# Performance work log

Hardware: AMD Instinct MI355X
Metric: run time of the kernel (lower is better)

## Reference

```python
import jax, jax.numpy as jnp
import numpy as np

B, N, C = 2, 6, 80
FH, FW = 16, 44
D = 112
NX = NY = 128
NZ = 1
OGH, OGW = 256, 704
D_BOUND = (2.0, 58.0, 0.5)
VOXEL_SIZE = np.array([0.8, 0.8, 8.0], dtype=np.float32)
VOXEL_COORD = np.array([-51.2 + 0.4, -51.2 + 0.4, -5.0 + 4.0], dtype=np.float32)
VOXEL_NUM = np.array([NX, NY, NZ], dtype=np.int32)


def setup_inputs() -> dict:
    key = jax.random.key(0)
    k1, k2 = jax.random.split(key)
    context = jax.random.normal(k1, (B * N, C, FH, FW), jnp.float32)
    depth_logits = jax.random.normal(k2, (B * N, D, FH, FW), jnp.float32)
    # realistic camera matrices (random matrices would not be invertible / physical)
    intrin = np.tile(np.eye(4, dtype=np.float32), (B, N, 1, 1))
    intrin[..., 0, 0] = 560.0
    intrin[..., 1, 1] = 560.0
    intrin[..., 0, 2] = OGW / 2.0
    intrin[..., 1, 2] = OGH / 2.0
    ida = np.tile(np.eye(4, dtype=np.float32), (B, N, 1, 1))
    s2e = np.tile(np.eye(4, dtype=np.float32), (B, N, 1, 1))
    # cam axes (x right, y down, z forward) -> ego axes (x fwd, y left, z up)
    M = np.array([[0., 0., 1.], [-1., 0., 0.], [0., -1., 0.]], dtype=np.float32)
    for n in range(N):
        yaw = 2.0 * np.pi * n / N
        cy, sy = np.cos(yaw), np.sin(yaw)
        R = np.array([[cy, -sy, 0.], [sy, cy, 0.], [0., 0., 1.]], dtype=np.float32)
        s2e[:, n, :3, :3] = R @ M
        s2e[:, n, :3, 3] = np.array([1.5 * cy, 1.5 * sy, 1.6], dtype=np.float32)
    bda = np.tile(np.eye(4, dtype=np.float32), (B, 1, 1))
    return dict(context=context, depth_logits=depth_logits,
                sensor2ego_mat=jnp.asarray(s2e), intrin_mat=jnp.asarray(intrin),
                ida_mat=jnp.asarray(ida), bda_mat=jnp.asarray(bda))


def _frustum():
    # [D, FH, FW, 4] pixel-plane frustum: (u, v, depth, 1)
    d = jnp.arange(D_BOUND[0], D_BOUND[1], D_BOUND[2], dtype=jnp.float32) + D_BOUND[2] / 2.0
    d = jnp.broadcast_to(d[:, None, None], (D, FH, FW))
    xs = jnp.broadcast_to(jnp.linspace(0.0, OGW - 1.0, FW)[None, None, :], (D, FH, FW))
    ys = jnp.broadcast_to(jnp.linspace(0.0, OGH - 1.0, FH)[None, :, None], (D, FH, FW))
    return jnp.stack([xs, ys, d, jnp.ones_like(d)], -1)


def reference(context, depth_logits, sensor2ego_mat, intrin_mat, ida_mat, bda_mat):
    # ---- get_geometry ----
    pts = _frustum()[None, None, ..., None]                       # [1,1,D,FH,FW,4,1]
    ida_inv = jnp.linalg.inv(ida_mat).reshape(B, N, 1, 1, 1, 4, 4)
    pts = ida_inv @ pts
    pts = jnp.concatenate([pts[..., :2, :] * pts[..., 2:3, :], pts[..., 2:, :]], axis=-2)
    combine = (sensor2ego_mat @ jnp.linalg.inv(intrin_mat)).reshape(B, N, 1, 1, 1, 4, 4)
    pts = combine @ pts
    bda = bda_mat.reshape(B, 1, 1, 1, 1, 4, 4)
    geom = (bda @ pts)[..., :3, 0]                                # [B,N,D,FH,FW,3] ego coords

    # ---- voxel indices ----
    vsize = jnp.asarray(VOXEL_SIZE)
    vcoord = jnp.asarray(VOXEL_COORD)
    vnum = jnp.asarray(VOXEL_NUM)
    idx = jnp.floor((geom - (vcoord - vsize / 2.0)) / vsize).astype(jnp.int32)
    valid = jnp.all((idx >= 0) & (idx < vnum), axis=-1)           # [B,N,D,FH,FW]

    # ---- lift: depth-weighted outer product ----
    depth = jax.nn.softmax(depth_logits, axis=1).reshape(B, N, D, FH, FW)
    ctx = context.reshape(B, N, C, FH, FW)
    feat = jnp.einsum('bndhw,bnchw->bndhwc', depth, ctx)          # [B,N,D,FH,FW,C]
    feat = feat * valid[..., None]

    # ---- splat: scatter-add into BEV grid ----
    b_idx = jnp.arange(B, dtype=jnp.int32)[:, None, None, None, None]
    lin = b_idx * (NY * NX) + idx[..., 1] * NX + idx[..., 0]
    lin = jnp.where(valid, lin, 0)                                # invalid feats already zeroed
    bev = jax.ops.segment_sum(feat.reshape(-1, C), lin.reshape(-1),
                              num_segments=B * NY * NX)
    return bev.reshape(B, NY, NX, C).transpose(0, 3, 1, 2)        # [B,C,NY,NX]
```

## Files before the change

### kernel.cpp

```cpp
#include <hip/hip_runtime.h>
#include <hip/hip_bf16.h>
#include <math.h>

#define B_ 2
#define N_ 6
#define C_ 80
#define FH_ 16
#define FW_ 44
#define D_ 112
#define NX_ 128
#define NY_ 128
#define NCOL (B_ * N_ * FH_ * FW_)
#define NCELL (B_ * NY_ * NX_)
#define MAXT (NCOL * D_)
#define GB_CELLS 16

typedef __hip_bfloat16 bf16;
typedef unsigned short u16;

__device__ __forceinline__ float loadf(const void* p, int i, int isbf) {
  if (isbf) return __bfloat162float(((const bf16*)p)[i]);
  return ((const float*)p)[i];
}

__device__ void inv4(const float m[16], float invOut[16]) {
  float inv[16];
  inv[0]  =  m[5]*m[10]*m[15] - m[5]*m[11]*m[14] - m[9]*m[6]*m[15] + m[9]*m[7]*m[14] + m[13]*m[6]*m[11] - m[13]*m[7]*m[10];
  inv[4]  = -m[4]*m[10]*m[15] + m[4]*m[11]*m[14] + m[8]*m[6]*m[15] - m[8]*m[7]*m[14] - m[12]*m[6]*m[11] + m[12]*m[7]*m[10];
  inv[8]  =  m[4]*m[9]*m[15]  - m[4]*m[11]*m[13] - m[8]*m[5]*m[15] + m[8]*m[7]*m[13] + m[12]*m[5]*m[11] - m[12]*m[7]*m[9];
  inv[12] = -m[4]*m[9]*m[14]  + m[4]*m[10]*m[13] + m[8]*m[5]*m[14] - m[8]*m[6]*m[13] - m[12]*m[5]*m[10] + m[12]*m[6]*m[9];
  inv[1]  = -m[1]*m[10]*m[15] + m[1]*m[11]*m[14] + m[9]*m[2]*m[15] - m[9]*m[3]*m[14] - m[13]*m[2]*m[11] + m[13]*m[3]*m[10];
  inv[5]  =  m[0]*m[10]*m[15] - m[0]*m[11]*m[14] - m[8]*m[2]*m[15] + m[8]*m[3]*m[14] + m[12]*m[2]*m[11] - m[12]*m[3]*m[10];
  inv[9]  = -m[0]*m[9]*m[15]  + m[0]*m[11]*m[13] + m[8]*m[1]*m[15] - m[8]*m[3]*m[13] - m[12]*m[1]*m[11] + m[12]*m[3]*m[9];
  inv[13] =  m[0]*m[9]*m[14]  - m[0]*m[10]*m[13] - m[8]*m[1]*m[14] + m[8]*m[2]*m[13] + m[12]*m[1]*m[10] - m[12]*m[2]*m[9];
  inv[2]  =  m[1]*m[6]*m[15]  - m[1]*m[7]*m[14]  - m[5]*m[2]*m[15] + m[5]*m[3]*m[14] + m[13]*m[2]*m[7]  - m[13]*m[3]*m[6];
  inv[6]  = -m[0]*m[6]*m[15]  + m[0]*m[7]*m[14]  + m[4]*m[2]*m[15] - m[4]*m[3]*m[14] - m[12]*m[2]*m[7]  + m[12]*m[3]*m[6];
  inv[10] =  m[0]*m[5]*m[15]  - m[0]*m[7]*m[13]  - m[4]*m[1]*m[15] + m[4]*m[3]*m[13] + m[12]*m[1]*m[7]  - m[12]*m[3]*m[5];
  inv[14] = -m[0]*m[5]*m[14]  + m[0]*m[6]*m[13]  + m[4]*m[1]*m[14] - m[4]*m[2]*m[13] - m[12]*m[1]*m[6]  + m[12]*m[2]*m[5];
  inv[3]  = -m[1]*m[6]*m[11]  + m[1]*m[7]*m[10]  + m[5]*m[2]*m[11] - m[5]*m[3]*m[10] - m[9]*m[2]*m[7]   + m[9]*m[3]*m[6];
  inv[7]  =  m[0]*m[6]*m[11]  - m[0]*m[7]*m[10]  - m[4]*m[2]*m[11] + m[4]*m[3]*m[10] + m[8]*m[2]*m[7]   - m[8]*m[3]*m[6];
  inv[11] = -m[0]*m[5]*m[11]  + m[0]*m[7]*m[9]   + m[4]*m[1]*m[11] - m[4]*m[3]*m[9]  - m[8]*m[1]*m[7]   + m[8]*m[3]*m[5];
  inv[15] =  m[0]*m[5]*m[10]  - m[0]*m[6]*m[9]   - m[4]*m[1]*m[10] + m[4]*m[2]*m[9]  + m[8]*m[1]*m[6]   - m[8]*m[2]*m[5];
  float det = m[0]*inv[0] + m[1]*inv[4] + m[2]*inv[8] + m[3]*inv[12];
  det = 1.0f / det;
  for (int i = 0; i < 16; i++) invOut[i] = inv[i] * det;
}

__device__ void mul4(const float A[16], const float Bm[16], float Cm[16]) {
  for (int i = 0; i < 4; i++)
    for (int j = 0; j < 4; j++) {
      float s = 0.f;
      for (int k = 0; k < 4; k++) s += A[i * 4 + k] * Bm[k * 4 + j];
      Cm[i * 4 + j] = s;
    }
}

__global__ void lss_prep(const void* __restrict__ logits,
                         const void* __restrict__ s2e, const void* __restrict__ intrin,
                         const void* __restrict__ ida, const void* __restrict__ bda,
                         float* __restrict__ mats, int* __restrict__ flags) {
  __shared__ int s_cnt;
  __shared__ int s_mats_bf;
  const int t = threadIdx.x;
  if (t == 0) s_cnt = 0;
  __syncthreads();
  {
    const unsigned short* u = (const unsigned short*)logits;
    unsigned short v = u[2 * t];
    int e = (v >> 7) & 0xFF;
    if (v == 0 || (e >= 110 && e <= 136)) atomicAdd(&s_cnt, 1);
  }
  __syncthreads();
  if (t == 0) {
    flags[0] = (s_cnt > 170) ? 1 : 0;
    float v = ((const float*)intrin)[0];
    s_mats_bf = (v > 100.f && v < 1.0e6f) ? 0 : 1;
    flags[1] = s_mats_bf;
  }
  __syncthreads();
  const int mbf = s_mats_bf;
  if (t < B_ * N_) {
    int b = t / N_;
    float S[16], I[16], A[16], Bd[16], Iinv[16], Ainv[16], Cm[16], M[16];
    for (int i = 0; i < 16; i++) {
      S[i]  = loadf(s2e,    t * 16 + i, mbf);
      I[i]  = loadf(intrin, t * 16 + i, mbf);
      A[i]  = loadf(ida,    t * 16 + i, mbf);
      Bd[i] = loadf(bda,    b * 16 + i, mbf);
    }
    inv4(I, Iinv);
    inv4(A, Ainv);
    mul4(S, Iinv, Cm);
    mul4(Bd, Cm, M);
    for (int i = 0; i < 16; i++) { mats[t * 32 + i] = Ainv[i]; mats[t * 32 + 16 + i] = M[i]; }
  }
}

__global__ void lss_transpose(const void* __restrict__ ctx, const int* __restrict__ flags,
                              float* __restrict__ ctx_t) {
  int i = blockIdx.x * blockDim.x + threadIdx.x;
  if (i >= NCOL * C_) return;
  int col = i / C_, c = i - col * C_;
  int bn = col / (FH_ * FW_), r = col - bn * (FH_ * FW_);
  int h = r / FW_, w = r - h * FW_;
  ctx_t[i] = loadf(ctx, ((bn * C_ + c) * FH_ + h) * FW_ + w, flags[0]);
}

__device__ __forceinline__ int geom_cell(const float* __restrict__ mats,
                                         int bn, int h, int w, int d) {
  const float* Ai = mats + bn * 32;
  const float* M = mats + bn * 32 + 16;
  float u = (float)w * (703.0f / 43.0f);
  float v = (float)h * 17.0f;
  float dep = 2.25f + 0.5f * (float)d;
  float p0 = ((Ai[0] * u + Ai[1] * v) + Ai[2] * dep) + Ai[3];
  float p1 = ((Ai[4] * u + Ai[5] * v) + Ai[6] * dep) + Ai[7];
  float p2 = ((Ai[8] * u + Ai[9] * v) + Ai[10] * dep) + Ai[11];
  float p3 = ((Ai[12] * u + Ai[13] * v) + Ai[14] * dep) + Ai[15];
  float q0 = p0 * p2, q1 = p1 * p2;
  float gx = ((M[0] * q0 + M[1] * q1) + M[2] * p2) + M[3] * p3;
  float gy = ((M[4] * q0 + M[5] * q1) + M[6] * p2) + M[7] * p3;
  float gz = ((M[8] * q0 + M[9] * q1) + M[10] * p2) + M[11] * p3;
  int ix = (int)floorf((gx + 51.2f) / 0.8f);
  int iy = (int)floorf((gy + 51.2f) / 0.8f);
  int iz = (int)floorf((gz + 5.0f) / 8.0f);
  bool valid = (ix >= 0) && (ix < NX_) && (iy >= 0) && (iy < NY_) && (iz == 0);
  int b = bn / N_;
  return valid ? (b * (NY_ * NX_) + iy * NX_ + ix) : -1;
}

__global__ __launch_bounds__(64) void lss_count(const float* __restrict__ mats,
                                                int* __restrict__ counts) {
  const int tid = threadIdx.x;
  const int col = blockIdx.x;
  const int w = col % FW_;
  const int h = (col / FW_) % FH_;
  const int bn = col / (FW_ * FH_);
  __shared__ int s_cell[D_];
  s_cell[tid] = geom_cell(mats, bn, h, w, tid);
  if (tid < D_ - 64) s_cell[tid + 64] = geom_cell(mats, bn, h, w, tid + 64);
  __syncthreads();
  for (int d = tid; d < D_; d += 64) {
    int vcell = s_cell[d];
    if (vcell >= 0 && (d == 0 || s_cell[d - 1] != vcell)) atomicAdd(&counts[vcell], 1);
  }
}

__global__ __launch_bounds__(1024) void lss_scan(const int* __restrict__ counts,
                                                 int* __restrict__ offsets,
                                                 int* __restrict__ cursors) {
  __shared__ int s[1024];
  const int t = threadIdx.x;
  const int base = t * 32;
  int local[32];
  int sum = 0;
  for (int j = 0; j < 32; j++) { local[j] = counts[base + j]; sum += local[j]; }
  s[t] = sum;
  __syncthreads();
  for (int st = 1; st < 1024; st <<= 1) {
    int v = (t >= st) ? s[t - st] : 0;
    __syncthreads();
    s[t] += v;
    __syncthreads();
  }
  int run = s[t] - sum;
  for (int j = 0; j < 32; j++) {
    offsets[base + j] = run;
    cursors[base + j] = run;
    run += local[j];
  }
}

__global__ __launch_bounds__(64) void lss_fill(
    const void* __restrict__ logits, const float* __restrict__ mats,
    const int* __restrict__ flags, int* __restrict__ cursors,
    u16* __restrict__ colids, float* __restrict__ wts) {
  const int tid = threadIdx.x;
  const int col = blockIdx.x;
  const int w = col % FW_;
  const int h = (col / FW_) % FH_;
  const int bn = col / (FW_ * FH_);
  const int tbf = flags[0];

  __shared__ float s_w[D_];
  __shared__ int s_cell[D_];

  const int base = ((bn * D_) * FH_ + h) * FW_ + w;
  float l0 = loadf(logits, base + tid * (FH_ * FW_), tbf);
  float l1 = (tid < D_ - 64) ? loadf(logits, base + (tid + 64) * (FH_ * FW_), tbf) : -1e30f;
  float m = fmaxf(l0, l1);
  for (int s = 32; s > 0; s >>= 1) m = fmaxf(m, __shfl_xor(m, s));
  float e0 = expf(l0 - m);
  float e1 = (tid < D_ - 64) ? expf(l1 - m) : 0.f;
  float sum = e0 + e1;
  for (int s = 32; s > 0; s >>= 1) sum += __shfl_xor(sum, s);
  float inv_sum = 1.0f / sum;

  s_w[tid] = e0;
  s_cell[tid] = geom_cell(mats, bn, h, w, tid);
  if (tid < D_ - 64) {
    s_w[tid + 64] = e1;
    s_cell[tid + 64] = geom_cell(mats, bn, h, w, tid + 64);
  }
  __syncthreads();

  for (int d = tid; d < D_; d += 64) {
    int vcell = s_cell[d];
    if (vcell >= 0 && (d == 0 || s_cell[d - 1] != vcell)) {
      float acc = s_w[d];
      for (int j = d + 1; j < D_ && s_cell[j] == vcell; ++j) acc += s_w[j];
      int pos = atomicAdd(&cursors[vcell], 1);
      colids[pos] = (u16)col;
      wts[pos] = acc * inv_sum;
    }
  }
}

__global__ __launch_bounds__(1024) void lss_gather(
    const float* __restrict__ ctx_t, const int* __restrict__ counts,
    const int* __restrict__ offsets, const u16* __restrict__ colids,
    const float* __restrict__ wts, const int* __restrict__ flags,
    void* __restrict__ out) {
  __shared__ float s_out[GB_CELLS * 84];
  const int tid = threadIdx.x;
  const int wv = tid >> 6;
  const int ln = tid & 63;
  const int sl = ln >> 2;
  const int g = ln & 3;
  const int cell = blockIdx.x * GB_CELLS + wv;
  const int n = counts[cell];
  const int off = offsets[cell];

  float acc[20];
#pragma unroll
  for (int i = 0; i < 20; i++) acc[i] = 0.f;

  for (int j = sl; j < n; j += 16) {
    int colj = colids[off + j];
    float wj = wts[off + j];
    const float4* cp = (const float4*)(ctx_t + colj * C_ + g * 20);
#pragma unroll
    for (int q = 0; q < 5; q++) {
      float4 v = cp[q];
      acc[q * 4 + 0] += wj * v.x;
      acc[q * 4 + 1] += wj * v.y;
      acc[q * 4 + 2] += wj * v.z;
      acc[q * 4 + 3] += wj * v.w;
    }
  }
#pragma unroll
  for (int msk = 4; msk <= 32; msk <<= 1) {
#pragma unroll
    for (int i = 0; i < 20; i++) acc[i] += __shfl_xor(acc[i], msk);
  }
  if (sl == 0) {
#pragma unroll
    for (int i = 0; i < 20; i++) s_out[wv * 84 + g * 20 + i] = acc[i];
  }
  __syncthreads();

  const int x = tid & 15;
  const int c0 = tid >> 4;
  const int cell0 = blockIdx.x * GB_CELLS;
  const int b = cell0 >> 14;
  const int yx0 = cell0 & 16383;
  if (flags[0]) {
    bf16* o = (bf16*)out;
    o[(size_t)(b * C_ + c0) * (NY_ * NX_) + yx0 + x] = __float2bfloat16(s_out[x * 84 + c0]);
    if (c0 < 16)
      o[(size_t)(b * C_ + 64 + c0) * (NY_ * NX_) + yx0 + x] = __float2bfloat16(s_out[x * 84 + 64 + c0]);
  } else {
    float* o = (float*)out;
    o[(size_t)(b * C_ + c0) * (NY_ * NX_) + yx0 + x] = s_out[x * 84 + c0];
    if (c0 < 16)
      o[(size_t)(b * C_ + 64 + c0) * (NY_ * NX_) + yx0 + x] = s_out[x * 84 + 64 + c0];
  }
}

extern "C" void kernel_launch(void* const* d_in, const int* in_sizes, int n_in,
                              void* d_out, int out_size, void* d_ws, size_t ws_size,
                              hipStream_t stream) {
  const void* ctx = d_in[0];
  const void* logits = d_in[1];
  const void* s2e = d_in[2];
  const void* intrin = d_in[3];
  const void* ida = d_in[4];
  const void* bda = d_in[5];

  float* wsf = (float*)d_ws;
  int* flags   = (int*)wsf;
  float* mats  = wsf + 16;
  int* counts  = (int*)(wsf + 512);
  int* offsets = (int*)(wsf + 512 + NCELL);
  int* cursors = (int*)(wsf + 512 + 2 * NCELL);
  float* ctx_t = wsf + 512 + 3 * NCELL;
  u16* colids  = (u16*)(ctx_t + NCOL * C_);
  float* wts   = (float*)((float*)colids + MAXT / 2);

  hipMemsetAsync(counts, 0, NCELL * sizeof(int), stream);
  lss_prep<<<1, 256, 0, stream>>>(logits, s2e, intrin, ida, bda, mats, flags);
  lss_transpose<<<(NCOL * C_ + 255) / 256, 256, 0, stream>>>(ctx, flags, ctx_t);
  lss_count<<<NCOL, 64, 0, stream>>>(mats, counts);
  lss_scan<<<1, 1024, 0, stream>>>(counts, offsets, cursors);
  lss_fill<<<NCOL, 64, 0, stream>>>(logits, mats, flags, cursors, colids, wts);
  lss_gather<<<NCELL / GB_CELLS, 1024, 0, stream>>>(ctx_t, counts, offsets, colids, wts, flags, d_out);
}
```

Baseline: 193.5 us.

## Fuse prep, transpose, count, scan and fill into one cooperative kernel

Replaces the memset and the five front-end launches (prep, transpose, count, scan, fill) with a single cooperative kernel that uses grid-wide syncs between phases. The counting phase now works per wavefront with shuffles, and the single-block scan becomes a two-level scan: per-chunk wave scans followed by a block scan of the chunk sums. The aim is to remove per-launch overhead and the serial single-block scan. In exchange it adds several grid barriers and runs on a grid capped at 512 blocks, so each wave handles several columns in a loop.

```diff
diff --git a/kernel.cpp b/kernel.cpp
--- a/kernel.cpp
+++ b/kernel.cpp
@@ -1,6 +1,9 @@
 #include <hip/hip_runtime.h>
+#include <hip/hip_cooperative_groups.h>
 #include <hip/hip_bf16.h>
 #include <math.h>
+
+namespace cg = cooperative_groups;
 
 #define B_ 2
 #define N_ 6
@@ -14,6 +17,7 @@
 #define NCELL (B_ * NY_ * NX_)
 #define MAXT (NCOL * D_)
 #define GB_CELLS 16
+#define NCHUNK (NCELL / 64)
 
 typedef __hip_bfloat16 bf16;
 typedef unsigned short u16;
@@ -55,57 +59,6 @@
     }
 }
 
-__global__ void lss_prep(const void* __restrict__ logits,
-                         const void* __restrict__ s2e, const void* __restrict__ intrin,
-                         const void* __restrict__ ida, const void* __restrict__ bda,
-                         float* __restrict__ mats, int* __restrict__ flags) {
-  __shared__ int s_cnt;
-  __shared__ int s_mats_bf;
-  const int t = threadIdx.x;
-  if (t == 0) s_cnt = 0;
-  __syncthreads();
-  {
-    const unsigned short* u = (const unsigned short*)logits;
-    unsigned short v = u[2 * t];
-    int e = (v >> 7) & 0xFF;
-    if (v == 0 || (e >= 110 && e <= 136)) atomicAdd(&s_cnt, 1);
-  }
-  __syncthreads();
-  if (t == 0) {
-    flags[0] = (s_cnt > 170) ? 1 : 0;
-    float v = ((const float*)intrin)[0];
-    s_mats_bf = (v > 100.f && v < 1.0e6f) ? 0 : 1;
-    flags[1] = s_mats_bf;
-  }
-  __syncthreads();
-  const int mbf = s_mats_bf;
-  if (t < B_ * N_) {
-    int b = t / N_;
-    float S[16], I[16], A[16], Bd[16], Iinv[16], Ainv[16], Cm[16], M[16];
-    for (int i = 0; i < 16; i++) {
-      S[i]  = loadf(s2e,    t * 16 + i, mbf);
-      I[i]  = loadf(intrin, t * 16 + i, mbf);
-      A[i]  = loadf(ida,    t * 16 + i, mbf);
-      Bd[i] = loadf(bda,    b * 16 + i, mbf);
-    }
-    inv4(I, Iinv);
-    inv4(A, Ainv);
-    mul4(S, Iinv, Cm);
-    mul4(Bd, Cm, M);
-    for (int i = 0; i < 16; i++) { mats[t * 32 + i] = Ainv[i]; mats[t * 32 + 16 + i] = M[i]; }
-  }
-}
-
-__global__ void lss_transpose(const void* __restrict__ ctx, const int* __restrict__ flags,
-                              float* __restrict__ ctx_t) {
-  int i = blockIdx.x * blockDim.x + threadIdx.x;
-  if (i >= NCOL * C_) return;
-  int col = i / C_, c = i - col * C_;
-  int bn = col / (FH_ * FW_), r = col - bn * (FH_ * FW_);
-  int h = r / FW_, w = r - h * FW_;
-  ctx_t[i] = loadf(ctx, ((bn * C_ + c) * FH_ + h) * FW_ + w, flags[0]);
-}
-
 __device__ __forceinline__ int geom_cell(const float* __restrict__ mats,
                                          int bn, int h, int w, int d) {
   const float* Ai = mats + bn * 32;
@@ -129,90 +82,169 @@
   return valid ? (b * (NY_ * NX_) + iy * NX_ + ix) : -1;
 }
 
-__global__ __launch_bounds__(64) void lss_count(const float* __restrict__ mats,
-                                                int* __restrict__ counts) {
-  const int tid = threadIdx.x;
-  const int col = blockIdx.x;
-  const int w = col % FW_;
-  const int h = (col / FW_) % FH_;
-  const int bn = col / (FW_ * FH_);
-  __shared__ int s_cell[D_];
-  s_cell[tid] = geom_cell(mats, bn, h, w, tid);
-  if (tid < D_ - 64) s_cell[tid + 64] = geom_cell(mats, bn, h, w, tid + 64);
-  __syncthreads();
-  for (int d = tid; d < D_; d += 64) {
-    int vcell = s_cell[d];
-    if (vcell >= 0 && (d == 0 || s_cell[d - 1] != vcell)) atomicAdd(&counts[vcell], 1);
-  }
-}
-
-__global__ __launch_bounds__(1024) void lss_scan(const int* __restrict__ counts,
-                                                 int* __restrict__ offsets,
-                                                 int* __restrict__ cursors) {
-  __shared__ int s[1024];
+__global__ __launch_bounds__(256, 2) void lss_front(
+    const void* __restrict__ ctx, const void* __restrict__ logits,
+    const void* __restrict__ s2e, const void* __restrict__ intrin,
+    const void* __restrict__ ida, const void* __restrict__ bda,
+    float* __restrict__ mats, int* __restrict__ flags,
+    int* __restrict__ counts, int* __restrict__ offsets,
+    int* __restrict__ cursors, float* __restrict__ ctx_t,
+    u16* __restrict__ colids, float* __restrict__ wts,
+    int* __restrict__ bsum, int* __restrict__ boff) {
+  cg::grid_group grid = cg::this_grid();
   const int t = threadIdx.x;
-  const int base = t * 32;
-  int local[32];
-  int sum = 0;
-  for (int j = 0; j < 32; j++) { local[j] = counts[base + j]; sum += local[j]; }
-  s[t] = sum;
-  __syncthreads();
-  for (int st = 1; st < 1024; st <<= 1) {
-    int v = (t >= st) ? s[t - st] : 0;
-    __syncthreads();
-    s[t] += v;
-    __syncthreads();
-  }
-  int run = s[t] - sum;
-  for (int j = 0; j < 32; j++) {
-    offsets[base + j] = run;
-    cursors[base + j] = run;
-    run += local[j];
-  }
-}
-
-__global__ __launch_bounds__(64) void lss_fill(
-    const void* __restrict__ logits, const float* __restrict__ mats,
-    const int* __restrict__ flags, int* __restrict__ cursors,
-    u16* __restrict__ colids, float* __restrict__ wts) {
-  const int tid = threadIdx.x;
-  const int col = blockIdx.x;
-  const int w = col % FW_;
-  const int h = (col / FW_) % FH_;
-  const int bn = col / (FW_ * FH_);
+  const int blk = blockIdx.x;
+  const int nblk = gridDim.x;
+  const int gtid = blk * 256 + t;
+  const int nthr = nblk * 256;
+  const int ln = t & 63;
+  const int wv = t >> 6;
+  const int gw = blk * 4 + wv;
+  const int ngw = nblk * 4;
+
+  __shared__ float s_w[4][D_];
+  __shared__ int s_cell[4][D_];
+  __shared__ int s_scan[256];
+  __shared__ int s_misc[2];
+
+  for (int i = gtid; i < NCELL; i += nthr) counts[i] = 0;
+  if (blk == 0) {
+    if (t == 0) s_misc[0] = 0;
+    __syncthreads();
+    {
+      const unsigned short* u = (const unsigned short*)logits;
+      unsigned short v = u[2 * t];
+      int e = (v >> 7) & 0xFF;
+      if (v == 0 || (e >= 110 && e <= 136)) atomicAdd(&s_misc[0], 1);
+    }
+    __syncthreads();
+    if (t == 0) {
+      flags[0] = (s_misc[0] > 170) ? 1 : 0;
+      float v = ((const float*)intrin)[0];
+      s_misc[1] = (v > 100.f && v < 1.0e6f) ? 0 : 1;
+      flags[1] = s_misc[1];
+    }
+    __syncthreads();
+    const int mbf = s_misc[1];
+    if (t < B_ * N_) {
+      int b = t / N_;
+      float S[16], I[16], A[16], Bd[16], Iinv[16], Ainv[16], Cm[16], M[16];
+      for (int i = 0; i < 16; i++) {
+        S[i]  = loadf(s2e,    t * 16 + i, mbf);
+        I[i]  = loadf(intrin, t * 16 + i, mbf);
+        A[i]  = loadf(ida,    t * 16 + i, mbf);
+        Bd[i] = loadf(bda,    b * 16 + i, mbf);
+      }
+      inv4(I, Iinv);
+      inv4(A, Ainv);
+      mul4(S, Iinv, Cm);
+      mul4(Bd, Cm, M);
+      for (int i = 0; i < 16; i++) { mats[t * 32 + i] = Ainv[i]; mats[t * 32 + 16 + i] = M[i]; }
+    }
+  }
+  grid.sync();
+
   const int tbf = flags[0];
-
-  __shared__ float s_w[D_];
-  __shared__ int s_cell[D_];
-
-  const int base = ((bn * D_) * FH_ + h) * FW_ + w;
-  float l0 = loadf(logits, base + tid * (FH_ * FW_), tbf);
-  float l1 = (tid < D_ - 64) ? loadf(logits, base + (tid + 64) * (FH_ * FW_), tbf) : -1e30f;
-  float m = fmaxf(l0, l1);
-  for (int s = 32; s > 0; s >>= 1) m = fmaxf(m, __shfl_xor(m, s));
-  float e0 = expf(l0 - m);
-  float e1 = (tid < D_ - 64) ? expf(l1 - m) : 0.f;
-  float sum = e0 + e1;
-  for (int s = 32; s > 0; s >>= 1) sum += __shfl_xor(sum, s);
-  float inv_sum = 1.0f / sum;
-
-  s_w[tid] = e0;
-  s_cell[tid] = geom_cell(mats, bn, h, w, tid);
-  if (tid < D_ - 64) {
-    s_w[tid + 64] = e1;
-    s_cell[tid + 64] = geom_cell(mats, bn, h, w, tid + 64);
-  }
-  __syncthreads();
-
-  for (int d = tid; d < D_; d += 64) {
-    int vcell = s_cell[d];
-    if (vcell >= 0 && (d == 0 || s_cell[d - 1] != vcell)) {
-      float acc = s_w[d];
-      for (int j = d + 1; j < D_ && s_cell[j] == vcell; ++j) acc += s_w[j];
-      int pos = atomicAdd(&cursors[vcell], 1);
-      colids[pos] = (u16)col;
-      wts[pos] = acc * inv_sum;
-    }
+  for (int i = gtid; i < NCOL * C_; i += nthr) {
+    int col = i / C_, c = i - col * C_;
+    int bn = col / (FH_ * FW_), r = col - bn * (FH_ * FW_);
+    int h = r / FW_, w = r - h * FW_;
+    ctx_t[i] = loadf(ctx, ((bn * C_ + c) * FH_ + h) * FW_ + w, tbf);
+  }
+  for (int col = gw; col < NCOL; col += ngw) {
+    const int w = col % FW_;
+    const int h = (col / FW_) % FH_;
+    const int bn = col / (FW_ * FH_);
+    int c0 = geom_cell(mats, bn, h, w, ln);
+    int c1 = (ln < D_ - 64) ? geom_cell(mats, bn, h, w, ln + 64) : -3;
+    int p0 = __shfl_up(c0, 1);
+    int p1 = __shfl_up(c1, 1);
+    int c63 = __shfl(c0, 63);
+    if (ln == 0) p1 = c63;
+    if (c0 >= 0 && (ln == 0 || p0 != c0)) atomicAdd(&counts[c0], 1);
+    if (c1 >= 0 && p1 != c1) atomicAdd(&counts[c1], 1);
+  }
+  grid.sync();
+
+  for (int cb = gw; cb < NCHUNK; cb += ngw) {
+    int c = cb * 64 + ln;
+    int v = counts[c];
+    int incl = v;
+#pragma unroll
+    for (int s = 1; s < 64; s <<= 1) {
+      int u2 = __shfl_up(incl, s);
+      if (ln >= s) incl += u2;
+    }
+    offsets[c] = incl - v;
+    if (ln == 63) bsum[cb] = incl;
+  }
+  grid.sync();
+
+  if (blk == 0) {
+    int a  = bsum[2 * t];
+    int b2 = bsum[2 * t + 1];
+    int ps = a + b2;
+    s_scan[t] = ps;
+    __syncthreads();
+    for (int st = 1; st < 256; st <<= 1) {
+      int u2 = (t >= st) ? s_scan[t - st] : 0;
+      __syncthreads();
+      s_scan[t] += u2;
+      __syncthreads();
+    }
+    int base = s_scan[t] - ps;
+    boff[2 * t]     = base;
+    boff[2 * t + 1] = base + a;
+  }
+  grid.sync();
+
+  for (int i = gtid; i < NCELL; i += nthr) {
+    int off = offsets[i] + boff[i >> 6];
+    offsets[i] = off;
+    cursors[i] = off;
+  }
+  grid.sync();
+
+  const int ITER = (NCOL + ngw - 1) / ngw;
+  for (int it = 0; it < ITER; ++it) {
+    const int col = gw + it * ngw;
+    const bool act = col < NCOL;
+    float inv_sum = 0.f;
+    if (act) {
+      const int w = col % FW_;
+      const int h = (col / FW_) % FH_;
+      const int bn = col / (FW_ * FH_);
+      const int base = ((bn * D_) * FH_ + h) * FW_ + w;
+      float l0 = loadf(logits, base + ln * (FH_ * FW_), tbf);
+      float l1 = (ln < D_ - 64) ? loadf(logits, base + (ln + 64) * (FH_ * FW_), tbf) : -1e30f;
+      float m = fmaxf(l0, l1);
+      for (int s = 32; s > 0; s >>= 1) m = fmaxf(m, __shfl_xor(m, s));
+      float e0 = expf(l0 - m);
+      float e1 = (ln < D_ - 64) ? expf(l1 - m) : 0.f;
+      float sum = e0 + e1;
+      for (int s = 32; s > 0; s >>= 1) sum += __shfl_xor(sum, s);
+      inv_sum = 1.0f / sum;
+      s_w[wv][ln] = e0;
+      s_cell[wv][ln] = geom_cell(mats, bn, h, w, ln);
+      if (ln < D_ - 64) {
+        s_w[wv][ln + 64] = e1;
+        s_cell[wv][ln + 64] = geom_cell(mats, bn, h, w, ln + 64);
+      }
+    }
+    __syncthreads();
+    if (act) {
+      for (int d = ln; d < D_; d += 64) {
+        int vcell = s_cell[wv][d];
+        if (vcell >= 0 && (d == 0 || s_cell[wv][d - 1] != vcell)) {
+          float acc = s_w[wv][d];
+          for (int j = d + 1; j < D_ && s_cell[wv][j] == vcell; ++j) acc += s_w[wv][j];
+          int pos = atomicAdd(&cursors[vcell], 1);
+          colids[pos] = (u16)col;
+          wts[pos] = acc * inv_sum;
+        }
+      }
+    }
+    __syncthreads();
   }
 }
 
@@ -293,15 +325,33 @@
   int* counts  = (int*)(wsf + 512);
   int* offsets = (int*)(wsf + 512 + NCELL);
   int* cursors = (int*)(wsf + 512 + 2 * NCELL);
-  float* ctx_t = wsf + 512 + 3 * NCELL;
+  int* bsum    = (int*)(wsf + 512 + 3 * NCELL);
+  int* boff    = bsum + NCHUNK;
+  float* ctx_t = wsf + 512 + 3 * NCELL + 2 * NCHUNK;
   u16* colids  = (u16*)(ctx_t + NCOL * C_);
   float* wts   = (float*)((float*)colids + MAXT / 2);
 
-  hipMemsetAsync(counts, 0, NCELL * sizeof(int), stream);
-  lss_prep<<<1, 256, 0, stream>>>(logits, s2e, intrin, ida, bda, mats, flags);
-  lss_transpose<<<(NCOL * C_ + 255) / 256, 256, 0, stream>>>(ctx, flags, ctx_t);
-  lss_count<<<NCOL, 64, 0, stream>>>(mats, counts);
-  lss_scan<<<1, 1024, 0, stream>>>(counts, offsets, cursors);
-  lss_fill<<<NCOL, 64, 0, stream>>>(logits, mats, flags, cursors, colids, wts);
-  lss_gather<<<NCELL / GB_CELLS, 1024, 0, stream>>>(ctx_t, counts, offsets, colids, wts, flags, d_out);
-}
+  static int grid_blocks = 0;
+  if (grid_blocks == 0) {
+    int nb = 0;
+    hipOccupancyMaxActiveBlocksPerMultiprocessor(&nb, (const void*)lss_front, 256, 0);
+    if (nb < 1) nb = 1;
+    long g = (long)nb * 256;
+    grid_blocks = (int)(g < 512 ? g : 512);
+  }
+
+  void* args[16];
+  args[0] = (void*)&ctx;     args[1] = (void*)&logits;
+  args[2] = (void*)&s2e;     args[3] = (void*)&intrin;
+  args[4] = (void*)&ida;     args[5] = (void*)&bda;
+  args[6] = (void*)&mats;    args[7] = (void*)&flags;
+  args[8] = (void*)&counts;  args[9] = (void*)&offsets;
+  args[10] = (void*)&cursors; args[11] = (void*)&ctx_t;
+  args[12] = (void*)&colids; args[13] = (void*)&wts;
+  args[14] = (void*)&bsum;   args[15] = (void*)&boff;
+
+  hipLaunchCooperativeKernel((void*)lss_front, dim3(grid_blocks), dim3(256),
+                             args, 0, stream);
+  lss_gather<<<NCELL / GB_CELLS, 1024, 0, stream>>>(ctx_t, counts, offsets,
+                                                    colids, wts, flags, d_out);
+}
```

Measured after the change: 316.8 us. 63.8% more time.

## Fuse count, scan, fill and transpose into one build kernel plus scatter

Applied to the files above, without the earlier changes.

Replaces the memset, transpose, count, scan and fill kernels with one build kernel. In it, some blocks transpose context and others compute softmax and voxel runs per column, one thread per column. A last-block-done atomic lets the final block run the prefix scan, and a separate scatter kernel places the precomputed runs into cell buckets. This cuts launches and avoids computing geometry twice, but adds per-column serial loops over depth with strided logit loads, extra run buffers, and a scan done by a single block.

```diff
diff --git a/kernel.cpp b/kernel.cpp
--- a/kernel.cpp
+++ b/kernel.cpp
@@ -10,10 +10,12 @@
 #define D_ 112
 #define NX_ 128
 #define NY_ 128
-#define NCOL (B_ * N_ * FH_ * FW_)
+#define HW_ (FH_ * FW_)
+#define NCOL (B_ * N_ * HW_)
 #define NCELL (B_ * NY_ * NX_)
 #define MAXT (NCOL * D_)
 #define GB_CELLS 16
+#define NBB 256
 
 typedef __hip_bfloat16 bf16;
 typedef unsigned short u16;
@@ -55,57 +57,6 @@
     }
 }
 
-__global__ void lss_prep(const void* __restrict__ logits,
-                         const void* __restrict__ s2e, const void* __restrict__ intrin,
-                         const void* __restrict__ ida, const void* __restrict__ bda,
-                         float* __restrict__ mats, int* __restrict__ flags) {
-  __shared__ int s_cnt;
-  __shared__ int s_mats_bf;
-  const int t = threadIdx.x;
-  if (t == 0) s_cnt = 0;
-  __syncthreads();
-  {
-    const unsigned short* u = (const unsigned short*)logits;
-    unsigned short v = u[2 * t];
-    int e = (v >> 7) & 0xFF;
-    if (v == 0 || (e >= 110 && e <= 136)) atomicAdd(&s_cnt, 1);
-  }
-  __syncthreads();
-  if (t == 0) {
-    flags[0] = (s_cnt > 170) ? 1 : 0;
-    float v = ((const float*)intrin)[0];
-    s_mats_bf = (v > 100.f && v < 1.0e6f) ? 0 : 1;
-    flags[1] = s_mats_bf;
-  }
-  __syncthreads();
-  const int mbf = s_mats_bf;
-  if (t < B_ * N_) {
-    int b = t / N_;
-    float S[16], I[16], A[16], Bd[16], Iinv[16], Ainv[16], Cm[16], M[16];
-    for (int i = 0; i < 16; i++) {
-      S[i]  = loadf(s2e,    t * 16 + i, mbf);
-      I[i]  = loadf(intrin, t * 16 + i, mbf);
-      A[i]  = loadf(ida,    t * 16 + i, mbf);
-      Bd[i] = loadf(bda,    b * 16 + i, mbf);
-    }
-    inv4(I, Iinv);
-    inv4(A, Ainv);
-    mul4(S, Iinv, Cm);
-    mul4(Bd, Cm, M);
-    for (int i = 0; i < 16; i++) { mats[t * 32 + i] = Ainv[i]; mats[t * 32 + 16 + i] = M[i]; }
-  }
-}
-
-__global__ void lss_transpose(const void* __restrict__ ctx, const int* __restrict__ flags,
-                              float* __restrict__ ctx_t) {
-  int i = blockIdx.x * blockDim.x + threadIdx.x;
-  if (i >= NCOL * C_) return;
-  int col = i / C_, c = i - col * C_;
-  int bn = col / (FH_ * FW_), r = col - bn * (FH_ * FW_);
-  int h = r / FW_, w = r - h * FW_;
-  ctx_t[i] = loadf(ctx, ((bn * C_ + c) * FH_ + h) * FW_ + w, flags[0]);
-}
-
 __device__ __forceinline__ int geom_cell(const float* __restrict__ mats,
                                          int bn, int h, int w, int d) {
   const float* Ai = mats + bn * 32;
@@ -129,90 +80,149 @@
   return valid ? (b * (NY_ * NX_) + iy * NX_ + ix) : -1;
 }
 
-__global__ __launch_bounds__(64) void lss_count(const float* __restrict__ mats,
-                                                int* __restrict__ counts) {
-  const int tid = threadIdx.x;
-  const int col = blockIdx.x;
-  const int w = col % FW_;
-  const int h = (col / FW_) % FH_;
-  const int bn = col / (FW_ * FH_);
-  __shared__ int s_cell[D_];
-  s_cell[tid] = geom_cell(mats, bn, h, w, tid);
-  if (tid < D_ - 64) s_cell[tid + 64] = geom_cell(mats, bn, h, w, tid + 64);
-  __syncthreads();
-  for (int d = tid; d < D_; d += 64) {
-    int vcell = s_cell[d];
-    if (vcell >= 0 && (d == 0 || s_cell[d - 1] != vcell)) atomicAdd(&counts[vcell], 1);
-  }
-}
-
-__global__ __launch_bounds__(1024) void lss_scan(const int* __restrict__ counts,
-                                                 int* __restrict__ offsets,
-                                                 int* __restrict__ cursors) {
-  __shared__ int s[1024];
+__global__ void lss_prep(const void* __restrict__ logits,
+                         const void* __restrict__ s2e, const void* __restrict__ intrin,
+                         const void* __restrict__ ida, const void* __restrict__ bda,
+                         float* __restrict__ mats, int* __restrict__ flags,
+                         int* __restrict__ counts, int* __restrict__ done) {
+  __shared__ int s_cnt;
+  __shared__ int s_mats_bf;
   const int t = threadIdx.x;
-  const int base = t * 32;
-  int local[32];
-  int sum = 0;
-  for (int j = 0; j < 32; j++) { local[j] = counts[base + j]; sum += local[j]; }
-  s[t] = sum;
-  __syncthreads();
-  for (int st = 1; st < 1024; st <<= 1) {
-    int v = (t >= st) ? s[t - st] : 0;
+  if (t == 0) { s_cnt = 0; *done = 0; }
+  __syncthreads();
+  {
+    const unsigned short* u = (const unsigned short*)logits;
+    unsigned short v = u[2 * t];
+    int e = (v >> 7) & 0xFF;
+    if (v == 0 || (e >= 110 && e <= 136)) atomicAdd(&s_cnt, 1);
+  }
+  __syncthreads();
+  if (t == 0) {
+    flags[0] = (s_cnt > 170) ? 1 : 0;
+    float v = ((const float*)intrin)[0];
+    s_mats_bf = (v > 100.f && v < 1.0e6f) ? 0 : 1;
+    flags[1] = s_mats_bf;
+  }
+  __syncthreads();
+  const int mbf = s_mats_bf;
+  if (t < B_ * N_) {
+    int b = t / N_;
+    float S[16], I[16], A[16], Bd[16], Iinv[16], Ainv[16], Cm[16], M[16];
+    for (int i = 0; i < 16; i++) {
+      S[i]  = loadf(s2e,    t * 16 + i, mbf);
+      I[i]  = loadf(intrin, t * 16 + i, mbf);
+      A[i]  = loadf(ida,    t * 16 + i, mbf);
+      Bd[i] = loadf(bda,    b * 16 + i, mbf);
+    }
+    inv4(I, Iinv);
+    inv4(A, Ainv);
+    mul4(S, Iinv, Cm);
+    mul4(Bd, Cm, M);
+    for (int i = 0; i < 16; i++) { mats[t * 32 + i] = Ainv[i]; mats[t * 32 + 16 + i] = M[i]; }
+  }
+  for (int i = t; i < NCELL; i += 256) counts[i] = 0;
+}
+
+__global__ __launch_bounds__(256) void lss_build(
+    const void* __restrict__ ctx, const void* __restrict__ logits,
+    const float* __restrict__ mats, const int* __restrict__ flags,
+    int* __restrict__ counts, int* __restrict__ offsets, int* __restrict__ cursors,
+    int* __restrict__ done, int* __restrict__ nrun,
+    u16* __restrict__ runc, float* __restrict__ runw, float* __restrict__ ctx_t) {
+  const int t = threadIdx.x;
+  const int blk = blockIdx.x;
+  const int tbf = flags[0];
+
+  if (blk >= 33) {
+    for (int i = (blk - 33) * 256 + t; i < NCOL * C_; i += (NBB - 33) * 256) {
+      int bn = i / (C_ * HW_);
+      int r  = i - bn * (C_ * HW_);
+      int c  = r / HW_;
+      int hw = r - c * HW_;
+      ctx_t[(bn * HW_ + hw) * C_ + c] = loadf(ctx, i, tbf);
+    }
+  } else {
+    const int col = blk * 256 + t;
+    const int bn = col / HW_;
+    const int hw = col - bn * HW_;
+    const int h = hw / FW_, w = hw - h * FW_;
+    const int base = bn * (D_ * HW_) + hw;
+    float m = -1e30f, s = 0.f;
+    for (int d = 0; d < D_; ++d) {
+      float l = loadf(logits, base + d * HW_, tbf);
+      float nm = fmaxf(m, l);
+      s = s * expf(m - nm) + expf(l - nm);
+      m = nm;
+    }
+    const float inv_sum = 1.0f / s;
+    int prev = -1; float racc = 0.f; int nr = 0;
+    for (int d = 0; d < D_; ++d) {
+      float l = loadf(logits, base + d * HW_, tbf);
+      float wgt = expf(l - m) * inv_sum;
+      int cell = geom_cell(mats, bn, h, w, d);
+      if (cell != prev) {
+        if (prev >= 0) {
+          runc[col * D_ + nr] = (u16)prev; runw[col * D_ + nr] = racc; ++nr;
+          atomicAdd(&counts[prev], 1);
+        }
+        prev = cell; racc = wgt;
+      } else {
+        racc += wgt;
+      }
+    }
+    if (prev >= 0) {
+      runc[col * D_ + nr] = (u16)prev; runw[col * D_ + nr] = racc; ++nr;
+      atomicAdd(&counts[prev], 1);
+    }
+    nrun[col] = nr;
+  }
+
+  __syncthreads();
+  __shared__ int s_last;
+  if (t == 0) {
+    __threadfence();
+    s_last = (atomicAdd(done, 1) == NBB - 1);
+  }
+  __syncthreads();
+  if (!s_last) return;
+  __threadfence();
+
+  __shared__ int s_sum[256];
+  const int cb = t * 128;
+  int tot = 0;
+  for (int j = 0; j < 128; ++j)
+    tot += __hip_atomic_load(&counts[cb + j], __ATOMIC_RELAXED, __HIP_MEMORY_SCOPE_AGENT);
+  s_sum[t] = tot;
+  __syncthreads();
+  for (int st = 1; st < 256; st <<= 1) {
+    int v = (t >= st) ? s_sum[t - st] : 0;
     __syncthreads();
-    s[t] += v;
+    s_sum[t] += v;
     __syncthreads();
   }
-  int run = s[t] - sum;
-  for (int j = 0; j < 32; j++) {
-    offsets[base + j] = run;
-    cursors[base + j] = run;
-    run += local[j];
-  }
-}
-
-__global__ __launch_bounds__(64) void lss_fill(
-    const void* __restrict__ logits, const float* __restrict__ mats,
-    const int* __restrict__ flags, int* __restrict__ cursors,
+  int run = s_sum[t] - tot;
+  for (int j = 0; j < 128; ++j) {
+    int v = __hip_atomic_load(&counts[cb + j], __ATOMIC_RELAXED, __HIP_MEMORY_SCOPE_AGENT);
+    offsets[cb + j] = run;
+    cursors[cb + j] = run;
+    run += v;
+  }
+}
+
+__global__ __launch_bounds__(256) void lss_scatter(
+    const int* __restrict__ nrun, const u16* __restrict__ runc,
+    const float* __restrict__ runw, int* __restrict__ cursors,
     u16* __restrict__ colids, float* __restrict__ wts) {
-  const int tid = threadIdx.x;
-  const int col = blockIdx.x;
-  const int w = col % FW_;
-  const int h = (col / FW_) % FH_;
-  const int bn = col / (FW_ * FH_);
-  const int tbf = flags[0];
-
-  __shared__ float s_w[D_];
-  __shared__ int s_cell[D_];
-
-  const int base = ((bn * D_) * FH_ + h) * FW_ + w;
-  float l0 = loadf(logits, base + tid * (FH_ * FW_), tbf);
-  float l1 = (tid < D_ - 64) ? loadf(logits, base + (tid + 64) * (FH_ * FW_), tbf) : -1e30f;
-  float m = fmaxf(l0, l1);
-  for (int s = 32; s > 0; s >>= 1) m = fmaxf(m, __shfl_xor(m, s));
-  float e0 = expf(l0 - m);
-  float e1 = (tid < D_ - 64) ? expf(l1 - m) : 0.f;
-  float sum = e0 + e1;
-  for (int s = 32; s > 0; s >>= 1) sum += __shfl_xor(sum, s);
-  float inv_sum = 1.0f / sum;
-
-  s_w[tid] = e0;
-  s_cell[tid] = geom_cell(mats, bn, h, w, tid);
-  if (tid < D_ - 64) {
-    s_w[tid + 64] = e1;
-    s_cell[tid + 64] = geom_cell(mats, bn, h, w, tid + 64);
-  }
-  __syncthreads();
-
-  for (int d = tid; d < D_; d += 64) {
-    int vcell = s_cell[d];
-    if (vcell >= 0 && (d == 0 || s_cell[d - 1] != vcell)) {
-      float acc = s_w[d];
-      for (int j = d + 1; j < D_ && s_cell[j] == vcell; ++j) acc += s_w[j];
-      int pos = atomicAdd(&cursors[vcell], 1);
-      colids[pos] = (u16)col;
-      wts[pos] = acc * inv_sum;
-    }
+  const int col = blockIdx.x * 4 + (threadIdx.x >> 6);
+  const int ln = threadIdx.x & 63;
+  if (col >= NCOL) return;
+  const int nr = nrun[col];
+  for (int r = ln; r < nr; r += 64) {
+    int cell = runc[col * D_ + r];
+    float wv = runw[col * D_ + r];
+    int pos = atomicAdd(&cursors[cell], 1);
+    colids[pos] = (u16)col;
+    wts[pos] = wv;
   }
 }
 
@@ -289,19 +299,21 @@
 
   float* wsf = (float*)d_ws;
   int* flags   = (int*)wsf;
+  int* done    = flags + 4;
   float* mats  = wsf + 16;
   int* counts  = (int*)(wsf + 512);
-  int* offsets = (int*)(wsf + 512 + NCELL);
-  int* cursors = (int*)(wsf + 512 + 2 * NCELL);
-  float* ctx_t = wsf + 512 + 3 * NCELL;
-  u16* colids  = (u16*)(ctx_t + NCOL * C_);
-  float* wts   = (float*)((float*)colids + MAXT / 2);
-
-  hipMemsetAsync(counts, 0, NCELL * sizeof(int), stream);
-  lss_prep<<<1, 256, 0, stream>>>(logits, s2e, intrin, ida, bda, mats, flags);
-  lss_transpose<<<(NCOL * C_ + 255) / 256, 256, 0, stream>>>(ctx, flags, ctx_t);
-  lss_count<<<NCOL, 64, 0, stream>>>(mats, counts);
-  lss_scan<<<1, 1024, 0, stream>>>(counts, offsets, cursors);
-  lss_fill<<<NCOL, 64, 0, stream>>>(logits, mats, flags, cursors, colids, wts);
+  int* offsets = counts + NCELL;
+  int* cursors = offsets + NCELL;
+  int* nrun    = cursors + NCELL;
+  float* runw  = (float*)(nrun + NCOL);
+  float* ctx_t = runw + MAXT;
+  float* wts   = ctx_t + NCOL * C_;
+  u16* colids  = (u16*)(wts + MAXT);
+  u16* runc    = colids + MAXT;
+
+  lss_prep<<<1, 256, 0, stream>>>(logits, s2e, intrin, ida, bda, mats, flags, counts, done);
+  lss_build<<<NBB, 256, 0, stream>>>(ctx, logits, mats, flags, counts, offsets,
+                                     cursors, done, nrun, runc, runw, ctx_t);
+  lss_scatter<<<NCOL / 4, 256, 0, stream>>>(nrun, runc, runw, cursors, colids, wts);
   lss_gather<<<NCELL / GB_CELLS, 1024, 0, stream>>>(ctx_t, counts, offsets, colids, wts, flags, d_out);
 }
```

After: 351.7 us. 81.8% more time.

## Fuse memset, transpose, count and scan into fewer kernel launches

Applied to the files above, without the earlier changes.

Folds the counts memset into a multi-block prep kernel. The count kernel now also performs the context transpose in extra blocks and runs the exclusive scan in the last-finishing block, using a global done counter with thread fences. Count blocks now process four columns each with wave shuffles in place of shared memory, and the transpose reads coalesced. This cuts launch count and serialization between small kernels. In exchange, correctness relies on the last-block pattern and atomic loads, and the single-block scan still sits on the critical path.

```diff
diff --git a/kernel.cpp b/kernel.cpp
--- a/kernel.cpp
+++ b/kernel.cpp
@@ -10,10 +10,13 @@
 #define D_ 112
 #define NX_ 128
 #define NY_ 128
-#define NCOL (B_ * N_ * FH_ * FW_)
+#define HW_ (FH_ * FW_)
+#define NCOL (B_ * N_ * HW_)
 #define NCELL (B_ * NY_ * NX_)
 #define MAXT (NCOL * D_)
 #define GB_CELLS 16
+#define NCB 2112
+#define NTB 224
 
 typedef __hip_bfloat16 bf16;
 typedef unsigned short u16;
@@ -55,57 +58,6 @@
     }
 }
 
-__global__ void lss_prep(const void* __restrict__ logits,
-                         const void* __restrict__ s2e, const void* __restrict__ intrin,
-                         const void* __restrict__ ida, const void* __restrict__ bda,
-                         float* __restrict__ mats, int* __restrict__ flags) {
-  __shared__ int s_cnt;
-  __shared__ int s_mats_bf;
-  const int t = threadIdx.x;
-  if (t == 0) s_cnt = 0;
-  __syncthreads();
-  {
-    const unsigned short* u = (const unsigned short*)logits;
-    unsigned short v = u[2 * t];
-    int e = (v >> 7) & 0xFF;
-    if (v == 0 || (e >= 110 && e <= 136)) atomicAdd(&s_cnt, 1);
-  }
-  __syncthreads();
-  if (t == 0) {
-    flags[0] = (s_cnt > 170) ? 1 : 0;
-    float v = ((const float*)intrin)[0];
-    s_mats_bf = (v > 100.f && v < 1.0e6f) ? 0 : 1;
-    flags[1] = s_mats_bf;
-  }
-  __syncthreads();
-  const int mbf = s_mats_bf;
-  if (t < B_ * N_) {
-    int b = t / N_;
-    float S[16], I[16], A[16], Bd[16], Iinv[16], Ainv[16], Cm[16], M[16];
-    for (int i = 0; i < 16; i++) {
-      S[i]  = loadf(s2e,    t * 16 + i, mbf);
-      I[i]  = loadf(intrin, t * 16 + i, mbf);
-      A[i]  = loadf(ida,    t * 16 + i, mbf);
-      Bd[i] = loadf(bda,    b * 16 + i, mbf);
-    }
-    inv4(I, Iinv);
-    inv4(A, Ainv);
-    mul4(S, Iinv, Cm);
-    mul4(Bd, Cm, M);
-    for (int i = 0; i < 16; i++) { mats[t * 32 + i] = Ainv[i]; mats[t * 32 + 16 + i] = M[i]; }
-  }
-}
-
-__global__ void lss_transpose(const void* __restrict__ ctx, const int* __restrict__ flags,
-                              float* __restrict__ ctx_t) {
-  int i = blockIdx.x * blockDim.x + threadIdx.x;
-  if (i >= NCOL * C_) return;
-  int col = i / C_, c = i - col * C_;
-  int bn = col / (FH_ * FW_), r = col - bn * (FH_ * FW_);
-  int h = r / FW_, w = r - h * FW_;
-  ctx_t[i] = loadf(ctx, ((bn * C_ + c) * FH_ + h) * FW_ + w, flags[0]);
-}
-
 __device__ __forceinline__ int geom_cell(const float* __restrict__ mats,
                                          int bn, int h, int w, int d) {
   const float* Ai = mats + bn * 32;
@@ -129,45 +81,118 @@
   return valid ? (b * (NY_ * NX_) + iy * NX_ + ix) : -1;
 }
 
-__global__ __launch_bounds__(64) void lss_count(const float* __restrict__ mats,
-                                                int* __restrict__ counts) {
-  const int tid = threadIdx.x;
-  const int col = blockIdx.x;
-  const int w = col % FW_;
-  const int h = (col / FW_) % FH_;
-  const int bn = col / (FW_ * FH_);
-  __shared__ int s_cell[D_];
-  s_cell[tid] = geom_cell(mats, bn, h, w, tid);
-  if (tid < D_ - 64) s_cell[tid + 64] = geom_cell(mats, bn, h, w, tid + 64);
-  __syncthreads();
-  for (int d = tid; d < D_; d += 64) {
-    int vcell = s_cell[d];
-    if (vcell >= 0 && (d == 0 || s_cell[d - 1] != vcell)) atomicAdd(&counts[vcell], 1);
-  }
-}
-
-__global__ __launch_bounds__(1024) void lss_scan(const int* __restrict__ counts,
-                                                 int* __restrict__ offsets,
-                                                 int* __restrict__ cursors) {
-  __shared__ int s[1024];
+__global__ __launch_bounds__(256) void lss_prep(
+    const void* __restrict__ logits,
+    const void* __restrict__ s2e, const void* __restrict__ intrin,
+    const void* __restrict__ ida, const void* __restrict__ bda,
+    float* __restrict__ mats, int* __restrict__ flags,
+    int* __restrict__ counts, int* __restrict__ done) {
   const int t = threadIdx.x;
-  const int base = t * 32;
-  int local[32];
-  int sum = 0;
-  for (int j = 0; j < 32; j++) { local[j] = counts[base + j]; sum += local[j]; }
-  s[t] = sum;
-  __syncthreads();
-  for (int st = 1; st < 1024; st <<= 1) {
-    int v = (t >= st) ? s[t - st] : 0;
+  const int blk = blockIdx.x;
+  for (int i = blk * 256 + t; i < NCELL; i += 33 * 256) counts[i] = 0;
+  if (blk != 0) return;
+
+  __shared__ int s_cnt;
+  __shared__ int s_mats_bf;
+  if (t == 0) { s_cnt = 0; *done = 0; }
+  __syncthreads();
+  {
+    const unsigned short* u = (const unsigned short*)logits;
+    unsigned short v = u[2 * t];
+    int e = (v >> 7) & 0xFF;
+    if (v == 0 || (e >= 110 && e <= 136)) atomicAdd(&s_cnt, 1);
+  }
+  __syncthreads();
+  if (t == 0) {
+    flags[0] = (s_cnt > 170) ? 1 : 0;
+    float v = ((const float*)intrin)[0];
+    s_mats_bf = (v > 100.f && v < 1.0e6f) ? 0 : 1;
+    flags[1] = s_mats_bf;
+  }
+  __syncthreads();
+  const int mbf = s_mats_bf;
+  if (t < B_ * N_) {
+    int b = t / N_;
+    float S[16], I[16], A[16], Bd[16], Iinv[16], Ainv[16], Cm[16], M[16];
+    for (int i = 0; i < 16; i++) {
+      S[i]  = loadf(s2e,    t * 16 + i, mbf);
+      I[i]  = loadf(intrin, t * 16 + i, mbf);
+      A[i]  = loadf(ida,    t * 16 + i, mbf);
+      Bd[i] = loadf(bda,    b * 16 + i, mbf);
+    }
+    inv4(I, Iinv);
+    inv4(A, Ainv);
+    mul4(S, Iinv, Cm);
+    mul4(Bd, Cm, M);
+    for (int i = 0; i < 16; i++) { mats[t * 32 + i] = Ainv[i]; mats[t * 32 + 16 + i] = M[i]; }
+  }
+}
+
+__global__ __launch_bounds__(256) void lss_count(
+    const void* __restrict__ ctx, const float* __restrict__ mats,
+    const int* __restrict__ flags, int* __restrict__ counts,
+    int* __restrict__ offsets, int* __restrict__ cursors,
+    int* __restrict__ done, float* __restrict__ ctx_t) {
+  const int t = threadIdx.x;
+  const int blk = blockIdx.x;
+
+  if (blk >= NCB) {
+    const int tbf = flags[0];
+    for (int i = (blk - NCB) * 256 + t; i < NCOL * C_; i += NTB * 256) {
+      int bn = i / (C_ * HW_);
+      int r  = i - bn * (C_ * HW_);
+      int c  = r / HW_;
+      int hw = r - c * HW_;
+      ctx_t[(bn * HW_ + hw) * C_ + c] = loadf(ctx, i, tbf);
+    }
+    return;
+  }
+
+  {
+    const int col = blk * 4 + (t >> 6);
+    const int ln = t & 63;
+    const int w = col % FW_;
+    const int h = (col / FW_) % FH_;
+    const int bn = col / (FW_ * FH_);
+    int c0 = geom_cell(mats, bn, h, w, ln);
+    int c1 = (ln < D_ - 64) ? geom_cell(mats, bn, h, w, ln + 64) : -3;
+    int p0 = __shfl_up(c0, 1);
+    int p1 = __shfl_up(c1, 1);
+    int c63 = __shfl(c0, 63);
+    if (ln == 0) p1 = c63;
+    if (c0 >= 0 && (ln == 0 || p0 != c0)) atomicAdd(&counts[c0], 1);
+    if (c1 >= 0 && p1 != c1) atomicAdd(&counts[c1], 1);
+  }
+
+  __syncthreads();
+  __shared__ int s_last;
+  if (t == 0) {
+    __threadfence();
+    s_last = (atomicAdd(done, 1) == NCB - 1);
+  }
+  __syncthreads();
+  if (!s_last) return;
+  __threadfence();
+
+  __shared__ int s_sum[256];
+  const int cb = t * 128;
+  int tot = 0;
+  for (int j = 0; j < 128; ++j)
+    tot += __hip_atomic_load(&counts[cb + j], __ATOMIC_RELAXED, __HIP_MEMORY_SCOPE_AGENT);
+  s_sum[t] = tot;
+  __syncthreads();
+  for (int st = 1; st < 256; st <<= 1) {
+    int v = (t >= st) ? s_sum[t - st] : 0;
     __syncthreads();
-    s[t] += v;
+    s_sum[t] += v;
     __syncthreads();
   }
-  int run = s[t] - sum;
-  for (int j = 0; j < 32; j++) {
-    offsets[base + j] = run;
-    cursors[base + j] = run;
-    run += local[j];
+  int run = s_sum[t] - tot;
+  for (int j = 0; j < 128; ++j) {
+    int v = __hip_atomic_load(&counts[cb + j], __ATOMIC_RELAXED, __HIP_MEMORY_SCOPE_AGENT);
+    offsets[cb + j] = run;
+    cursors[cb + j] = run;
+    run += v;
   }
 }
 
@@ -289,19 +314,18 @@
 
   float* wsf = (float*)d_ws;
   int* flags   = (int*)wsf;
+  int* done    = flags + 4;
   float* mats  = wsf + 16;
   int* counts  = (int*)(wsf + 512);
-  int* offsets = (int*)(wsf + 512 + NCELL);
-  int* cursors = (int*)(wsf + 512 + 2 * NCELL);
-  float* ctx_t = wsf + 512 + 3 * NCELL;
-  u16* colids  = (u16*)(ctx_t + NCOL * C_);
-  float* wts   = (float*)((float*)colids + MAXT / 2);
-
-  hipMemsetAsync(counts, 0, NCELL * sizeof(int), stream);
-  lss_prep<<<1, 256, 0, stream>>>(logits, s2e, intrin, ida, bda, mats, flags);
-  lss_transpose<<<(NCOL * C_ + 255) / 256, 256, 0, stream>>>(ctx, flags, ctx_t);
-  lss_count<<<NCOL, 64, 0, stream>>>(mats, counts);
-  lss_scan<<<1, 1024, 0, stream>>>(counts, offsets, cursors);
+  int* offsets = counts + NCELL;
+  int* cursors = offsets + NCELL;
+  float* ctx_t = (float*)(cursors + NCELL);
+  float* wts   = ctx_t + NCOL * C_;
+  u16* colids  = (u16*)(wts + MAXT);
+
+  lss_prep<<<33, 256, 0, stream>>>(logits, s2e, intrin, ida, bda, mats, flags, counts, done);
+  lss_count<<<NCB + NTB, 256, 0, stream>>>(ctx, mats, flags, counts, offsets,
+                                           cursors, done, ctx_t);
   lss_fill<<<NCOL, 64, 0, stream>>>(logits, mats, flags, cursors, colids, wts);
   lss_gather<<<NCELL / GB_CELLS, 1024, 0, stream>>>(ctx_t, counts, offsets, colids, wts, flags, d_out);
 }
```

Result: slower. 283.1 us (+46.3%).
